# Kernel optimization log

Measured on AMD Instinct MI355X. Metric: run time of the kernel, lower is better.

## Reference

```python
import jax, jax.numpy as jnp
import numpy as np
from jax import lax

PAIRS = ((0, 1), (1, 2), (2, 3), (3, 0))


def _apply_1q(state, U, w):
    # state: (N,2,2,2,2); wire w lives at axis w+1
    state = jnp.moveaxis(state, w + 1, -1)
    if U.ndim == 2:  # shared gate across batch
        state = jnp.einsum('ij,...j->...i', U, state)
    else:            # per-batch gate (encoder), U: (N,2,2)
        state = jnp.einsum('nij,n...j->n...i', U, state)
    return jnp.moveaxis(state, -1, w + 1)


def _ry_mat(theta):
    # torchquantum RY: [[cos(t/2), -sin(t/2)], [sin(t/2), cos(t/2)]]
    h = theta * 0.5
    c, s = jnp.cos(h), jnp.sin(h)
    return jnp.stack([jnp.stack([c, -s], -1), jnp.stack([s, c], -1)], -2).astype(jnp.complex64)


def _rz_mat(theta):
    # torchquantum RZ: diag(e^{-i t/2}, e^{+i t/2})
    h = (theta * 0.5).astype(jnp.complex64)
    e0, e1 = jnp.exp(-1j * h), jnp.exp(1j * h)
    z = jnp.zeros_like(e0)
    return jnp.stack([jnp.stack([e0, z], -1), jnp.stack([z, e1], -1)], -2)


def _cnot(state, c, t):
    st = jnp.moveaxis(state, (c + 1, t + 1), (-2, -1))
    st = jnp.stack([st[..., 0, :], st[..., 1, ::-1]], axis=-2)
    return jnp.moveaxis(st, (-2, -1), (c + 1, t + 1))


def _ansatz(state, p, a, b):
    state = _apply_1q(state, _ry_mat(p[0]), a)
    state = _apply_1q(state, _rz_mat(p[1]), a)
    state = _apply_1q(state, _ry_mat(p[2]), b)
    state = _apply_1q(state, _rz_mat(p[3]), b)
    state = _cnot(state, a, b)
    state = _apply_1q(state, _ry_mat(p[4]), a)
    state = _apply_1q(state, _rz_mat(p[5]), a)
    state = _apply_1q(state, _ry_mat(p[6]), b)
    return state


def _circuit(angles, qp):
    # angles: (N,4) in [0,pi]; qp: (2,7). Returns <Z_w> per wire: (N,4)
    N = angles.shape[0]
    state = jnp.zeros((N, 2, 2, 2, 2), jnp.complex64).at[:, 0, 0, 0, 0].set(1.0)
    for w in range(4):  # GeneralEncoder: RY(x_w) on wire w
        state = _apply_1q(state, _ry_mat(angles[:, w]), w)
    for layer in range(2):
        for (a, b) in PAIRS:
            state = _ansatz(state, qp[layer], a, b)
    probs = state.real ** 2 + state.imag ** 2
    exps = []
    for w in range(4):
        axes = tuple(ax for ax in range(1, 5) if ax != w + 1)
        m = probs.sum(axis=axes)  # (N,2)
        exps.append(m[:, 0] - m[:, 1])
    return jnp.stack(exps, axis=-1)


def _conv(x, w, b):
    y = lax.conv_general_dilated(x, w, (1, 1), 'SAME',
                                 dimension_numbers=('NCHW', 'OIHW', 'NCHW'))
    return y + b[None, :, None, None]


def _pool(x):
    return lax.reduce_window(x, -jnp.inf, lax.max, (1, 1, 2, 2), (1, 1, 2, 2), 'VALID')


def setup_inputs() -> dict:
    key = jax.random.key(0)
    ks = jax.random.split(key, 16)
    r = lambda k, sh, sc=0.1: (jax.random.normal(k, sh, dtype=jnp.float32) * sc)
    return {
        'x': jax.random.normal(ks[0], (2048, 1, 28, 28), dtype=jnp.float32),
        'conv1_w': r(ks[1], (64, 1, 3, 3)), 'conv1_b': r(ks[2], (64,)),
        'conv2_w': r(ks[3], (16, 64, 3, 3)), 'conv2_b': r(ks[4], (16,)),
        'conv3_w': r(ks[5], (4, 16, 3, 3)), 'conv3_b': r(ks[6], (4,)),
        'q_params': jax.random.uniform(ks[7], (2, 7), dtype=jnp.float32),
        'fc1_w': r(ks[8], (64, 196)), 'fc1_b': r(ks[9], (64,)),
        'fc2_w': r(ks[10], (128, 64)), 'fc2_b': r(ks[11], (128,)),
        'fc3_w': r(ks[12], (64, 128)), 'fc3_b': r(ks[13], (64,)),
        'fc4_w': r(ks[14], (10, 64)), 'fc4_b': r(ks[15], (10,)),
    }


def reference(x, conv1_w, conv1_b, conv2_w, conv2_b, conv3_w, conv3_b,
              q_params, fc1_w, fc1_b, fc2_w, fc2_b, fc3_w, fc3_b, fc4_w, fc4_b):
    h = _pool(jax.nn.relu(_conv(x, conv1_w, conv1_b)))       # (B,64,14,14)
    h = _pool(jax.nn.relu(_conv(h, conv2_w, conv2_b)))       # (B,16,7,7)
    h = jax.nn.leaky_relu(_conv(h, conv3_w, conv3_b), 0.01)  # (B,4,7,7)
    B, C, H, W = h.shape
    # 1x1 patches: (B, H*W, C) -> flatten over patches
    patches = h.reshape(B, C, H * W).transpose(0, 2, 1).reshape(B * H * W, C)
    angles = jax.nn.sigmoid(patches) * np.float32(np.pi)
    q = _circuit(angles, q_params)            # (B*49, 4)
    q = q.reshape(B, H * W * C)               # (B, 196)
    h = jax.nn.relu(q @ fc1_w.T + fc1_b)
    h = h @ fc2_w.T + fc2_b
    h = jax.nn.relu(h @ fc3_w.T + fc3_b)
    return h @ fc4_w.T + fc4_b
```

## Files before the change

### kernel.cpp

```cpp
#include <hip/hip_runtime.h>
#include <hip/hip_bf16.h>
#include <math.h>

#define DEV __device__ __forceinline__

typedef __attribute__((ext_vector_type(4))) float f32x4;
typedef __attribute__((ext_vector_type(8))) short bf16x8;

DEV unsigned short f2bf(float v) {
    __hip_bfloat16 h = __float2bfloat16(v);
    return *reinterpret_cast<unsigned short*>(&h);
}
DEV unsigned pk2(float a, float b) {
    union { __hip_bfloat162 b2; unsigned u; } cv;
    cv.b2 = __float22bfloat162_rn(float2{a, b});
    return cv.u;
}

template<int B>
DEV void ry_b(float* sr, float* si, float c, float s) {
    #pragma unroll
    for (int i = 0; i < 16; ++i) if (!(i & B)) {
        int j = i | B;
        float r0 = sr[i], m0 = si[i], r1 = sr[j], m1 = si[j];
        sr[i] = c * r0 - s * r1;  si[i] = c * m0 - s * m1;
        sr[j] = s * r0 + c * r1;  si[j] = s * m0 + c * m1;
    }
}
template<int B>
DEV void rz_b(float* sr, float* si, float c, float s) {
    #pragma unroll
    for (int i = 0; i < 16; ++i) {
        float xr = sr[i], xi = si[i];
        if (!(i & B)) { sr[i] = c * xr + s * xi;  si[i] = c * xi - s * xr; }
        else          { sr[i] = c * xr - s * xi;  si[i] = c * xi + s * xr; }
    }
}
template<int BC, int BT>
DEV void cnot_b(float* sr, float* si) {
    #pragma unroll
    for (int i = 0; i < 16; ++i) if ((i & BC) && !(i & BT)) {
        int j = i | BT;
        float tr = sr[i]; sr[i] = sr[j]; sr[j] = tr;
        float ti = si[i]; si[i] = si[j]; si[j] = ti;
    }
}
template<int A, int Bw>
DEV void ansatz(float* sr, float* si, const float* cc, const float* ss) {
    constexpr int BA = 8 >> A, BB = 8 >> Bw;
    ry_b<BA>(sr, si, cc[0], ss[0]);
    rz_b<BA>(sr, si, cc[1], ss[1]);
    ry_b<BB>(sr, si, cc[2], ss[2]);
    rz_b<BB>(sr, si, cc[3], ss[3]);
    cnot_b<BA, BB>(sr, si);
    ry_b<BA>(sr, si, cc[4], ss[4]);
    rz_b<BA>(sr, si, cc[5], ss[5]);
    ry_b<BB>(sr, si, cc[6], ss[6]);
}

__global__ void prep_kernel(const float* __restrict__ w1,
                            const float* __restrict__ w2,
                            const float* __restrict__ w3,
                            const float* __restrict__ qp,
                            const float* __restrict__ fc1w,
                            const float* __restrict__ fc2w,
                            const float* __restrict__ fc3w,
                            const float* __restrict__ fc4w,
                            unsigned short* __restrict__ w1b,
                            unsigned short* __restrict__ w2b,
                            float* __restrict__ w3t,
                            float* __restrict__ ab,
                            float* __restrict__ fc1t,
                            float* __restrict__ fc2t,
                            float* __restrict__ fc3t,
                            float* __restrict__ fc4t)
{
    int t = blockIdx.x * blockDim.x + threadIdx.x;
    int NT = gridDim.x * blockDim.x;
    for (int i = t; i < 2048; i += NT) {
        int j = i & 7, oc = (i >> 3) & 63, fqq = i >> 9;
        int tap = fqq * 8 + j;
        w1b[i] = tap < 9 ? f2bf(w1[oc * 9 + tap]) : (unsigned short)0;
    }
    for (int i = t; i < 9216; i += NT) {
        int j = i & 7, oc = (i >> 3) & 15, fq = (i >> 7) & 3, f = i >> 9;
        int tap = f >> 1, kk = f & 1;
        int s = kk * 32 + fq * 8 + j;
        int ic = (s & 3) * 16 + (s >> 2);
        w2b[i] = f2bf(w2[(oc * 64 + ic) * 9 + tap]);
    }
    for (int i = t; i < 576; i += NT) {
        int c = i & 3, ch = (i >> 2) & 15, tap = i >> 6;
        w3t[i] = w3[(c * 16 + ch) * 9 + tap];
    }
    for (int i = t; i < 12544; i += NT) { int j = i / 196, k = i % 196; fc1t[k * 64 + j] = fc1w[i]; }
    for (int i = t; i < 8192;  i += NT) { int j = i / 64,  k = i % 64;  fc2t[k * 128 + j] = fc2w[i]; }
    for (int i = t; i < 8192;  i += NT) { int j = i / 128, k = i % 128; fc3t[k * 64 + j] = fc3w[i]; }
    for (int i = t; i < 640;   i += NT) { int j = i / 64,  k = i % 64;  fc4t[k * 10 + j] = fc4w[i]; }

    if (blockIdx.x == 0 && threadIdx.x < 16) {
        int b = threadIdx.x;
        float cs0[7], sn0[7], cs1[7], sn1[7];
        #pragma unroll
        for (int k = 0; k < 7; ++k) {
            __sincosf(qp[k] * 0.5f, &sn0[k], &cs0[k]);
            __sincosf(qp[7 + k] * 0.5f, &sn1[k], &cs1[k]);
        }
        float sr[16], si[16];
        #pragma unroll
        for (int i = 0; i < 16; ++i) { sr[i] = (i == b) ? 1.f : 0.f; si[i] = 0.f; }
        ansatz<0, 1>(sr, si, cs0, sn0);
        ansatz<1, 2>(sr, si, cs0, sn0);
        ansatz<2, 3>(sr, si, cs0, sn0);
        ansatz<3, 0>(sr, si, cs0, sn0);
        ansatz<0, 1>(sr, si, cs1, sn1);
        ansatz<1, 2>(sr, si, cs1, sn1);
        ansatz<2, 3>(sr, si, cs1, sn1);
        ansatz<3, 0>(sr, si, cs1, sn1);
        #pragma unroll
        for (int i = 0; i < 16; ++i) {
            ab[(i * 16 + b) * 2]     = sr[i];
            ab[(i * 16 + b) * 2 + 1] = si[i];
        }
    }
}

__global__ __launch_bounds__(256, 4) void conv12_kernel(
    const float* __restrict__ x,
    const float* __restrict__ b1, const unsigned short* __restrict__ w1b,
    const unsigned short* __restrict__ w2b,
    const float* __restrict__ b2, float* __restrict__ out2)
{
    __shared__ __align__(128) char lds_all[36864];
    float* pin = (float*)lds_all;
    char* in_b = lds_all + 4096;
    int t = threadIdx.x, lane = t & 63, wv = t >> 6;
    int fq = lane >> 4, fr = lane & 15;
    int n = blockIdx.x;

    bf16x8 bfrag[18];
    const bf16x8* wb = (const bf16x8*)w2b;
    #pragma unroll
    for (int f = 0; f < 18; ++f) bfrag[f] = wb[(f * 4 + fq) * 16 + fr];
    bf16x8 w1f[4];
    const bf16x8* wb1 = (const bf16x8*)w1b;
    float b1v[4];
    #pragma unroll
    for (int nt = 0; nt < 4; ++nt) {
        w1f[nt] = wb1[fq * 64 + nt * 16 + fr];
        b1v[nt] = b1[nt * 16 + fr];
    }
    float b2v = b2[fr];

    for (int i = t; i < 480; i += 256) {
        int ci = i >> 3, sub = i & 7;
        int g;
        if (ci < 16)      g = ci;
        else if (ci < 32) g = 240 + (ci - 16);
        else if (ci < 46) g = (ci - 31) * 16;
        else              g = (ci - 45) * 16 + 15;
        *(f32x4*)(in_b + g * 128 + sub * 16) = f32x4{0.f, 0.f, 0.f, 0.f};
    }
    if (t < 124) {
        int row, col;
        if (t < 68) { row = (t < 34) ? 0 : 29; col = (t < 34) ? t : t - 34; }
        else {
            int j = t - 68;
            if (j < 28) { row = j + 1;  col = 0; }
            else        { row = j - 27; col = 29; }
        }
        pin[row * 34 + col] = 0.f;
    }
    if (t >= 124 && t < 252) {
        int tt = t - 124;
        int cell = tt >> 2, comp = tt & 3;
        int pos;
        if (cell < 9)       pos = cell;
        else if (cell < 18) pos = 72 + (cell - 9);
        else if (cell < 25) pos = (cell - 17) * 9;
        else                pos = (cell - 24) * 9 + 8;
        *reinterpret_cast<float4*>(out2 + (size_t)n * 1296 + pos * 16 + comp * 4)
            = float4{0.f, 0.f, 0.f, 0.f};
    }
    for (int i = t; i < 784; i += 256) pin[(i / 28 + 1) * 34 + (i % 28) + 1] = x[n * 784 + i];
    __syncthreads();

    for (int tile = wv; tile < 49; tile += 4) {
        int pooledA = tile * 4 + (fr >> 2);
        int pyA = pooledA / 14, pxA = pooledA - pyA * 14;
        int Y = 2 * pyA + ((fr >> 1) & 1), X = 2 * pxA + (fr & 1);
        const float* ap = pin + Y * 34 + X + (fq == 1 ? 70 : 0);
        float q0 = ap[0],  q1 = ap[1],  q2 = ap[2];
        float q3 = ap[34], q4 = ap[35], q5 = ap[36];
        float q6 = ap[68], q7 = ap[69];
        union { uint4 u; bf16x8 v; } A;
        A.u.x = pk2(q0, q1); A.u.y = pk2(q2, q3);
        A.u.z = pk2(q4, q5); A.u.w = pk2(q6, q7);

        f32x4 a0 = {0.f,0.f,0.f,0.f}, a1 = {0.f,0.f,0.f,0.f},
              a2 = {0.f,0.f,0.f,0.f}, a3 = {0.f,0.f,0.f,0.f};
        a0 = __builtin_amdgcn_mfma_f32_16x16x32_bf16(A.v, w1f[0], a0, 0, 0, 0);
        a1 = __builtin_amdgcn_mfma_f32_16x16x32_bf16(A.v, w1f[1], a1, 0, 0, 0);
        a2 = __builtin_amdgcn_mfma_f32_16x16x32_bf16(A.v, w1f[2], a2, 0, 0, 0);
        a3 = __builtin_amdgcn_mfma_f32_16x16x32_bf16(A.v, w1f[3], a3, 0, 0, 0);

        int pooled = tile * 4 + fq;
        int py = pooled / 14, px = pooled - py * 14;
        int grid = (py + 1) * 16 + (px + 1);
        unsigned swz = (unsigned)(grid & 7) << 4;
        float v0 = fmaxf(fmaxf(fmaxf(a0[0], a0[1]), fmaxf(a0[2], a0[3])) + b1v[0], 0.f);
        float v1 = fmaxf(fmaxf(fmaxf(a1[0], a1[1]), fmaxf(a1[2], a1[3])) + b1v[1], 0.f);
        float v2 = fmaxf(fmaxf(fmaxf(a2[0], a2[1]), fmaxf(a2[2], a2[3])) + b1v[2], 0.f);
        float v3 = fmaxf(fmaxf(fmaxf(a3[0], a3[1]), fmaxf(a3[2], a3[3])) + b1v[3], 0.f);
        uint2 w; w.x = pk2(v0, v1); w.y = pk2(v2, v3);
        *reinterpret_cast<uint2*>(in_b + (((unsigned)grid * 128 + (unsigned)fr * 8) ^ swz)) = w;
    }
    __syncthreads();

    for (int tile = wv; tile < 13; tile += 4) {
        f32x4 acc = {0.f, 0.f, 0.f, 0.f};
        int pv = tile * 4 + (fr >> 2); pv = pv > 48 ? 48 : pv;
        int sub = fr & 3;
        int y7 = pv / 7, x7 = pv - y7 * 7;
        int y = 2 * y7 + (sub >> 1), xx = 2 * x7 + (sub & 1);
        int g0 = y * 16 + xx;
        int vb = g0 * 128 + fq * 16;
        #pragma unroll
        for (int ky = 0; ky < 3; ++ky)
            #pragma unroll
            for (int kx = 0; kx < 3; ++kx) {
                int dg = ky * 16 + kx;
                int msk = ((g0 + dg) & 7) << 4;
                int lin = vb + dg * 128;
                bf16x8 a0 = *(const bf16x8*)(in_b + (lin ^ msk));
                acc = __builtin_amdgcn_mfma_f32_16x16x32_bf16(a0, bfrag[(ky * 3 + kx) * 2], acc, 0, 0, 0);
                bf16x8 a1 = *(const bf16x8*)(in_b + ((lin | 64) ^ msk));
                acc = __builtin_amdgcn_mfma_f32_16x16x32_bf16(a1, bfrag[(ky * 3 + kx) * 2 + 1], acc, 0, 0, 0);
            }
        int pooled2 = tile * 4 + fq;
        if (pooled2 < 49) {
            float m = fmaxf(fmaxf(acc[0], acc[1]), fmaxf(acc[2], acc[3]));
            int y9 = pooled2 / 7, x9 = pooled2 - y9 * 7;
            out2[(size_t)n * 1296 + ((y9 + 1) * 9 + (x9 + 1)) * 16 + fr] =
                fmaxf(m + b2v, 0.f);
        }
    }
}

__global__ __launch_bounds__(512) void qfc_kernel(
    const float* __restrict__ out2, const float* __restrict__ w3t,
    const float* __restrict__ b3, const float* __restrict__ ab,
    const float* __restrict__ fc1t, const float* __restrict__ fb1,
    const float* __restrict__ fc2t, const float* __restrict__ fb2,
    const float* __restrict__ fc3t, const float* __restrict__ fb3,
    const float* __restrict__ fc4t, const float* __restrict__ fb4,
    float* __restrict__ out)
{
    __shared__ float qr[8][196];
    __shared__ float h1[8][64], h2[8][128], h3[8][64];
    int t = threadIdx.x;
    int nb = blockIdx.x * 8;

    if (t < 392) {
        int nl = t / 49, p = t - nl * 49;
        int n = nb + nl;
        int py = p / 7, px = p - py * 7;
        const float* in = out2 + (size_t)n * 1296;

        float acc0 = b3[0], acc1 = b3[1], acc2 = b3[2], acc3 = b3[3];
        #pragma unroll
        for (int ky = 0; ky < 3; ++ky)
            #pragma unroll
            for (int kx = 0; kx < 3; ++kx) {
                const float* cp = in + ((py + ky) * 9 + (px + kx)) * 16;
                const float* wt = w3t + (ky * 3 + kx) * 64;
                #pragma unroll
                for (int icq = 0; icq < 4; ++icq) {
                    float4 v4 = *reinterpret_cast<const float4*>(cp + icq * 4);
                    const float* wq = wt + icq * 16;
                    acc0 = fmaf(wq[0],  v4.x, acc0); acc1 = fmaf(wq[1],  v4.x, acc1);
                    acc2 = fmaf(wq[2],  v4.x, acc2); acc3 = fmaf(wq[3],  v4.x, acc3);
                    acc0 = fmaf(wq[4],  v4.y, acc0); acc1 = fmaf(wq[5],  v4.y, acc1);
                    acc2 = fmaf(wq[6],  v4.y, acc2); acc3 = fmaf(wq[7],  v4.y, acc3);
                    acc0 = fmaf(wq[8],  v4.z, acc0); acc1 = fmaf(wq[9],  v4.z, acc1);
                    acc2 = fmaf(wq[10], v4.z, acc2); acc3 = fmaf(wq[11], v4.z, acc3);
                    acc0 = fmaf(wq[12], v4.w, acc0); acc1 = fmaf(wq[13], v4.w, acc1);
                    acc2 = fmaf(wq[14], v4.w, acc2); acc3 = fmaf(wq[15], v4.w, acc3);
                }
            }

        float cw[4], sw[4];
        {
            float az[4] = {acc0, acc1, acc2, acc3};
            #pragma unroll
            for (int c = 0; c < 4; ++c) {
                float z = az[c];
                z = z > 0.f ? z : 0.01f * z;
                float sg = 1.f / (1.f + __expf(-z));
                __sincosf(1.5707963267948966f * sg, &sw[c], &cw[c]);
            }
        }
        float p01[4] = { cw[0]*cw[1], cw[0]*sw[1], sw[0]*cw[1], sw[0]*sw[1] };
        float p23[4] = { cw[2]*cw[3], cw[2]*sw[3], sw[2]*cw[3], sw[2]*sw[3] };
        float v[16];
        #pragma unroll
        for (int i = 0; i < 16; ++i) v[i] = p01[i >> 2] * p23[i & 3];

        float e0 = 0.f, e1 = 0.f, e2 = 0.f, e3 = 0.f;
        #pragma unroll
        for (int i = 0; i < 16; ++i) {
            const float* row = ab + i * 32;
            float re = 0.f, im = 0.f;
            #pragma unroll
            for (int k = 0; k < 16; ++k) {
                re = fmaf(row[k * 2],     v[k], re);
                im = fmaf(row[k * 2 + 1], v[k], im);
            }
            float p2 = re * re + im * im;
            e0 += (i & 8) ? -p2 : p2;
            e1 += (i & 4) ? -p2 : p2;
            e2 += (i & 2) ? -p2 : p2;
            e3 += (i & 1) ? -p2 : p2;
        }
        *reinterpret_cast<float4*>(&qr[nl][p * 4]) = float4{e0, e1, e2, e3};
    }
    __syncthreads();

    int wv = t >> 6, lane = t & 63;
    int n = nb + wv;
    float a = fb1[lane];
    for (int k = 0; k < 196; ++k) a = fmaf(fc1t[k * 64 + lane], qr[wv][k], a);
    h1[wv][lane] = fmaxf(a, 0.f);
    __syncthreads();
    float a0 = fb2[lane], a1 = fb2[lane + 64];
    for (int k = 0; k < 64; ++k) {
        float vv = h1[wv][k];
        a0 = fmaf(fc2t[k * 128 + lane], vv, a0);
        a1 = fmaf(fc2t[k * 128 + lane + 64], vv, a1);
    }
    h2[wv][lane] = a0; h2[wv][lane + 64] = a1;
    __syncthreads();
    a = fb3[lane];
    for (int k = 0; k < 128; ++k) a = fmaf(fc3t[k * 64 + lane], h2[wv][k], a);
    h3[wv][lane] = fmaxf(a, 0.f);
    __syncthreads();
    if (lane < 10) {
        a = fb4[lane];
        for (int k = 0; k < 64; ++k) a = fmaf(fc4t[k * 10 + lane], h3[wv][k], a);
        out[n * 10 + lane] = a;
    }
}

extern "C" void kernel_launch(void* const* d_in, const int* in_sizes, int n_in,
                              void* d_out, int out_size, void* d_ws, size_t ws_size,
                              hipStream_t stream) {
    const float* x      = (const float*)d_in[0];
    const float* c1w    = (const float*)d_in[1];
    const float* c1b    = (const float*)d_in[2];
    const float* c2w    = (const float*)d_in[3];
    const float* c2b    = (const float*)d_in[4];
    const float* c3w    = (const float*)d_in[5];
    const float* c3b    = (const float*)d_in[6];
    const float* qp     = (const float*)d_in[7];
    const float* fc1w   = (const float*)d_in[8];
    const float* fc1b   = (const float*)d_in[9];
    const float* fc2w   = (const float*)d_in[10];
    const float* fc2b   = (const float*)d_in[11];
    const float* fc3w   = (const float*)d_in[12];
    const float* fc3b   = (const float*)d_in[13];
    const float* fc4w   = (const float*)d_in[14];
    const float* fc4b   = (const float*)d_in[15];
    float* out = (float*)d_out;

    float* ws = (float*)d_ws;
    unsigned short* w2b = (unsigned short*)ws;
    unsigned short* w1b = (unsigned short*)(ws + 4608);
    float* w3t  = ws + 5632;
    float* abm  = ws + 6208;
    float* fc1t = ws + 6720;
    float* fc2t = fc1t + 12544;
    float* fc3t = fc2t + 8192;
    float* fc4t = fc3t + 8192;
    float* out2 = fc4t + 640;

    prep_kernel<<<40, 256, 0, stream>>>(c1w, c2w, c3w, qp, fc1w, fc2w, fc3w, fc4w,
                                        w1b, w2b, w3t, abm, fc1t, fc2t, fc3t, fc4t);
    conv12_kernel<<<2048, 256, 0, stream>>>(x, c1b, w1b, w2b, c2b, out2);
    qfc_kernel<<<256, 512, 0, stream>>>(out2, w3t, c3b, abm,
                                        fc1t, fc1b, fc2t, fc2b,
                                        fc3t, fc3b, fc4t, fc4b, out);
}
```

Baseline: 63.59 us.

## Restructure qfc kernel to one sample per block with split-K FC layers

The qfc kernel now runs one sample per 256-thread block (2048 blocks) instead of eight samples per 512-thread block (256 blocks). Conv3 is split per output channel, the quantum expectation rows are split four ways across threads, and each FC layer is split along K across four waves with a shared-memory reduction. The aim is more parallelism and occupancy across the GPU in the tail kernel. In exchange it adds more barriers and repeats the FC weight reads once per sample block.

```diff
diff --git a/kernel.cpp b/kernel.cpp
--- a/kernel.cpp
+++ b/kernel.cpp
@@ -68,7 +68,7 @@
                             const float* __restrict__ fc4w,
                             unsigned short* __restrict__ w1b,
                             unsigned short* __restrict__ w2b,
-                            float* __restrict__ w3t,
+                            float* __restrict__ w3c,
                             float* __restrict__ ab,
                             float* __restrict__ fc1t,
                             float* __restrict__ fc2t,
@@ -90,8 +90,8 @@
         w2b[i] = f2bf(w2[(oc * 64 + ic) * 9 + tap]);
     }
     for (int i = t; i < 576; i += NT) {
-        int c = i & 3, ch = (i >> 2) & 15, tap = i >> 6;
-        w3t[i] = w3[(c * 16 + ch) * 9 + tap];
+        int ic = i & 15, tap = (i >> 4) % 9, c = i / 144;
+        w3c[i] = w3[(c * 16 + ic) * 9 + tap];
     }
     for (int i = t; i < 12544; i += NT) { int j = i / 196, k = i % 196; fc1t[k * 64 + j] = fc1w[i]; }
     for (int i = t; i < 8192;  i += NT) { int j = i / 64,  k = i % 64;  fc2t[k * 128 + j] = fc2w[i]; }
@@ -247,8 +247,8 @@
     }
 }
 
-__global__ __launch_bounds__(512) void qfc_kernel(
-    const float* __restrict__ out2, const float* __restrict__ w3t,
+__global__ __launch_bounds__(256, 4) void qfc_kernel(
+    const float* __restrict__ out2, const float* __restrict__ w3c,
     const float* __restrict__ b3, const float* __restrict__ ab,
     const float* __restrict__ fc1t, const float* __restrict__ fb1,
     const float* __restrict__ fc2t, const float* __restrict__ fb2,
@@ -256,59 +256,59 @@
     const float* __restrict__ fc4t, const float* __restrict__ fb4,
     float* __restrict__ out)
 {
-    __shared__ float qr[8][196];
-    __shared__ float h1[8][64], h2[8][128], h3[8][64];
-    int t = threadIdx.x;
-    int nb = blockIdx.x * 8;
-
-    if (t < 392) {
-        int nl = t / 49, p = t - nl * 49;
-        int n = nb + nl;
+    __shared__ float2 cwsw[196];
+    __shared__ float4 part[196];
+    __shared__ __align__(16) float qr[196];
+    __shared__ float red[4][128];
+    __shared__ float h1[64], h2[128], h3[64];
+    int t = threadIdx.x, wv = t >> 6, lane = t & 63;
+    int n = blockIdx.x;
+    const float* in = out2 + (size_t)n * 1296;
+
+    if (t < 196) {
+        int p = t >> 2, c = t & 3;
         int py = p / 7, px = p - py * 7;
-        const float* in = out2 + (size_t)n * 1296;
-
-        float acc0 = b3[0], acc1 = b3[1], acc2 = b3[2], acc3 = b3[3];
+        float acc = b3[c];
         #pragma unroll
         for (int ky = 0; ky < 3; ++ky)
             #pragma unroll
             for (int kx = 0; kx < 3; ++kx) {
                 const float* cp = in + ((py + ky) * 9 + (px + kx)) * 16;
-                const float* wt = w3t + (ky * 3 + kx) * 64;
+                const float* wp = w3c + (c * 9 + ky * 3 + kx) * 16;
                 #pragma unroll
                 for (int icq = 0; icq < 4; ++icq) {
-                    float4 v4 = *reinterpret_cast<const float4*>(cp + icq * 4);
-                    const float* wq = wt + icq * 16;
-                    acc0 = fmaf(wq[0],  v4.x, acc0); acc1 = fmaf(wq[1],  v4.x, acc1);
-                    acc2 = fmaf(wq[2],  v4.x, acc2); acc3 = fmaf(wq[3],  v4.x, acc3);
-                    acc0 = fmaf(wq[4],  v4.y, acc0); acc1 = fmaf(wq[5],  v4.y, acc1);
-                    acc2 = fmaf(wq[6],  v4.y, acc2); acc3 = fmaf(wq[7],  v4.y, acc3);
-                    acc0 = fmaf(wq[8],  v4.z, acc0); acc1 = fmaf(wq[9],  v4.z, acc1);
-                    acc2 = fmaf(wq[10], v4.z, acc2); acc3 = fmaf(wq[11], v4.z, acc3);
-                    acc0 = fmaf(wq[12], v4.w, acc0); acc1 = fmaf(wq[13], v4.w, acc1);
-                    acc2 = fmaf(wq[14], v4.w, acc2); acc3 = fmaf(wq[15], v4.w, acc3);
+                    float4 dv  = *reinterpret_cast<const float4*>(cp + icq * 4);
+                    float4 wv4 = *reinterpret_cast<const float4*>(wp + icq * 4);
+                    acc = fmaf(wv4.x, dv.x, acc);
+                    acc = fmaf(wv4.y, dv.y, acc);
+                    acc = fmaf(wv4.z, dv.z, acc);
+                    acc = fmaf(wv4.w, dv.w, acc);
                 }
             }
-
-        float cw[4], sw[4];
-        {
-            float az[4] = {acc0, acc1, acc2, acc3};
-            #pragma unroll
-            for (int c = 0; c < 4; ++c) {
-                float z = az[c];
-                z = z > 0.f ? z : 0.01f * z;
-                float sg = 1.f / (1.f + __expf(-z));
-                __sincosf(1.5707963267948966f * sg, &sw[c], &cw[c]);
-            }
-        }
-        float p01[4] = { cw[0]*cw[1], cw[0]*sw[1], sw[0]*cw[1], sw[0]*sw[1] };
-        float p23[4] = { cw[2]*cw[3], cw[2]*sw[3], sw[2]*cw[3], sw[2]*sw[3] };
+        float z = acc > 0.f ? acc : 0.01f * acc;
+        float sg = 1.f / (1.f + __expf(-z));
+        float sv, cv;
+        __sincosf(1.5707963267948966f * sg, &sv, &cv);
+        cwsw[t] = float2{cv, sv};
+    }
+    __syncthreads();
+
+    if (t < 196) {
+        int p = t >> 2, qd = t & 3;
+        float2 c0 = cwsw[p * 4 + 0];
+        float2 c1 = cwsw[p * 4 + 1];
+        float2 c2 = cwsw[p * 4 + 2];
+        float2 c3 = cwsw[p * 4 + 3];
+        float p01[4] = { c0.x*c1.x, c0.x*c1.y, c0.y*c1.x, c0.y*c1.y };
+        float p23[4] = { c2.x*c3.x, c2.x*c3.y, c2.y*c3.x, c2.y*c3.y };
         float v[16];
         #pragma unroll
         for (int i = 0; i < 16; ++i) v[i] = p01[i >> 2] * p23[i & 3];
 
         float e0 = 0.f, e1 = 0.f, e2 = 0.f, e3 = 0.f;
         #pragma unroll
-        for (int i = 0; i < 16; ++i) {
+        for (int ii = 0; ii < 4; ++ii) {
+            int i = qd * 4 + ii;
             const float* row = ab + i * 32;
             float re = 0.f, im = 0.f;
             #pragma unroll
@@ -322,33 +322,74 @@
             e2 += (i & 2) ? -p2 : p2;
             e3 += (i & 1) ? -p2 : p2;
         }
-        *reinterpret_cast<float4*>(&qr[nl][p * 4]) = float4{e0, e1, e2, e3};
-    }
-    __syncthreads();
-
-    int wv = t >> 6, lane = t & 63;
-    int n = nb + wv;
-    float a = fb1[lane];
-    for (int k = 0; k < 196; ++k) a = fmaf(fc1t[k * 64 + lane], qr[wv][k], a);
-    h1[wv][lane] = fmaxf(a, 0.f);
-    __syncthreads();
-    float a0 = fb2[lane], a1 = fb2[lane + 64];
-    for (int k = 0; k < 64; ++k) {
-        float vv = h1[wv][k];
-        a0 = fmaf(fc2t[k * 128 + lane], vv, a0);
-        a1 = fmaf(fc2t[k * 128 + lane + 64], vv, a1);
-    }
-    h2[wv][lane] = a0; h2[wv][lane + 64] = a1;
-    __syncthreads();
-    a = fb3[lane];
-    for (int k = 0; k < 128; ++k) a = fmaf(fc3t[k * 64 + lane], h2[wv][k], a);
-    h3[wv][lane] = fmaxf(a, 0.f);
-    __syncthreads();
+        part[t] = float4{e0, e1, e2, e3};
+    }
+    __syncthreads();
+
+    if (t < 49) {
+        float4 s0 = part[t * 4 + 0], s1 = part[t * 4 + 1];
+        float4 s2 = part[t * 4 + 2], s3 = part[t * 4 + 3];
+        float4 r;
+        r.x = (s0.x + s1.x) + (s2.x + s3.x);
+        r.y = (s0.y + s1.y) + (s2.y + s3.y);
+        r.z = (s0.z + s1.z) + (s2.z + s3.z);
+        r.w = (s0.w + s1.w) + (s2.w + s3.w);
+        *reinterpret_cast<float4*>(&qr[t * 4]) = r;
+    }
+    __syncthreads();
+
+    {
+        float s = 0.f;
+        int k0 = 49 * wv;
+        for (int k = 0; k < 49; ++k)
+            s = fmaf(fc1t[(k0 + k) * 64 + lane], qr[k0 + k], s);
+        red[wv][lane] = s;
+    }
+    __syncthreads();
+    if (wv == 0)
+        h1[lane] = fmaxf(fb1[lane] + ((red[0][lane] + red[1][lane]) + (red[2][lane] + red[3][lane])), 0.f);
+    __syncthreads();
+
+    {
+        float s0 = 0.f, s1 = 0.f;
+        int k0 = 16 * wv;
+        for (int k = 0; k < 16; ++k) {
+            float v = h1[k0 + k];
+            s0 = fmaf(fc2t[(k0 + k) * 128 + lane],      v, s0);
+            s1 = fmaf(fc2t[(k0 + k) * 128 + lane + 64], v, s1);
+        }
+        red[wv][lane]      = s0;
+        red[wv][lane + 64] = s1;
+    }
+    __syncthreads();
+    if (wv == 0) {
+        h2[lane]      = fb2[lane]      + ((red[0][lane] + red[1][lane]) + (red[2][lane] + red[3][lane]));
+        h2[lane + 64] = fb2[lane + 64] + ((red[0][lane + 64] + red[1][lane + 64]) + (red[2][lane + 64] + red[3][lane + 64]));
+    }
+    __syncthreads();
+
+    {
+        float s = 0.f;
+        int k0 = 32 * wv;
+        for (int k = 0; k < 32; ++k)
+            s = fmaf(fc3t[(k0 + k) * 64 + lane], h2[k0 + k], s);
+        red[wv][lane] = s;
+    }
+    __syncthreads();
+    if (wv == 0)
+        h3[lane] = fmaxf(fb3[lane] + ((red[0][lane] + red[1][lane]) + (red[2][lane] + red[3][lane])), 0.f);
+    __syncthreads();
+
     if (lane < 10) {
-        a = fb4[lane];
-        for (int k = 0; k < 64; ++k) a = fmaf(fc4t[k * 10 + lane], h3[wv][k], a);
-        out[n * 10 + lane] = a;
-    }
+        float s = 0.f;
+        int k0 = 16 * wv;
+        for (int k = 0; k < 16; ++k)
+            s = fmaf(fc4t[(k0 + k) * 10 + lane], h3[k0 + k], s);
+        red[wv][lane] = s;
+    }
+    __syncthreads();
+    if (t < 10)
+        out[(size_t)n * 10 + t] = fb4[t] + ((red[0][t] + red[1][t]) + (red[2][t] + red[3][t]));
 }
 
 extern "C" void kernel_launch(void* const* d_in, const int* in_sizes, int n_in,
@@ -375,7 +416,7 @@
     float* ws = (float*)d_ws;
     unsigned short* w2b = (unsigned short*)ws;
     unsigned short* w1b = (unsigned short*)(ws + 4608);
-    float* w3t  = ws + 5632;
+    float* w3c  = ws + 5632;
     float* abm  = ws + 6208;
     float* fc1t = ws + 6720;
     float* fc2t = fc1t + 12544;
@@ -384,9 +425,9 @@
     float* out2 = fc4t + 640;
 
     prep_kernel<<<40, 256, 0, stream>>>(c1w, c2w, c3w, qp, fc1w, fc2w, fc3w, fc4w,
-                                        w1b, w2b, w3t, abm, fc1t, fc2t, fc3t, fc4t);
+                                        w1b, w2b, w3c, abm, fc1t, fc2t, fc3t, fc4t);
     conv12_kernel<<<2048, 256, 0, stream>>>(x, c1b, w1b, w2b, c2b, out2);
-    qfc_kernel<<<256, 512, 0, stream>>>(out2, w3t, c3b, abm,
-                                        fc1t, fc1b, fc2t, fc2b,
-                                        fc3t, fc3b, fc4t, fc4b, out);
-}
+    qfc_kernel<<<2048, 256, 0, stream>>>(out2, w3c, c3b, abm,
+                                         fc1t, fc1b, fc2t, fc2b,
+                                         fc3t, fc3b, fc4t, fc4b, out);
+}
```

New measurement: 94.31 us. +48.3%, slower.
